# Performance work log

Measured on AMD Instinct MI355X. Metric: run time of the kernel, lower is better.

Reference implementation:

```python
import jax, jax.numpy as jnp
import numpy as np

B, I, D = 2048, 4096, 512          # batch of candidates, num rated items, item_dim
IE, UE = 512, 1024                 # item_emb, user_emb
D1, D2, D3 = 1024, 512, 256        # MLP dense widths


def setup_inputs() -> dict:
    key = jax.random.key(0)
    ks = jax.random.split(key, 16)
    s = 0.02  # weight init scale
    candidate_items = jax.random.normal(ks[0], (B, D), dtype=jnp.float32)
    rated_items = jax.random.normal(ks[1], (I, D), dtype=jnp.float32)
    ratings = jax.random.uniform(ks[2], (B, I), dtype=jnp.float32, minval=0.5, maxval=5.0)
    keep = jax.random.uniform(ks[3], (B, I)) < 0.05
    user_matrix = jnp.where(keep, ratings, 0.0)
    return dict(
        candidate_items=candidate_items,
        rated_items=rated_items,
        user_matrix=user_matrix,
        att_w=jax.random.normal(ks[4], (2 * D, 1), dtype=jnp.float32) * s,
        att_b=jnp.zeros((1,), jnp.float32),
        iw1=jax.random.normal(ks[5], (D, 2 * IE), dtype=jnp.float32) * s,
        ib1=jnp.zeros((2 * IE,), jnp.float32),
        iw2=jax.random.normal(ks[6], (2 * IE, IE), dtype=jnp.float32) * s,
        ib2=jnp.zeros((IE,), jnp.float32),
        uw1=jax.random.normal(ks[7], (D, 2 * UE), dtype=jnp.float32) * s,
        ub1=jnp.zeros((2 * UE,), jnp.float32),
        uw2=jax.random.normal(ks[8], (2 * UE, UE), dtype=jnp.float32) * s,
        ub2=jnp.zeros((UE,), jnp.float32),
        mw1=jax.random.normal(ks[9], (IE + UE, D1), dtype=jnp.float32) * s,
        mb1=jnp.zeros((D1,), jnp.float32),
        mw2=jax.random.normal(ks[10], (D1, D2), dtype=jnp.float32) * s,
        mb2=jnp.zeros((D2,), jnp.float32),
        mw3=jax.random.normal(ks[11], (D2, D3), dtype=jnp.float32) * s,
        mb3=jnp.zeros((D3,), jnp.float32),
        mw4=jax.random.normal(ks[12], (D3, 1), dtype=jnp.float32) * s,
        mb4=jnp.zeros((1,), jnp.float32),
    )


def reference(candidate_items, rated_items, user_matrix,
              att_w, att_b, iw1, ib1, iw2, ib2, uw1, ub1, uw2, ub2,
              mw1, mb1, mw2, mb2, mw3, mb3, mw4, mb4):
    d = candidate_items.shape[1]
    # AttentionNet(Linear(2D,1)) on cat(cand_repeat, rated_tile) decomposes exactly:
    # score[b,i] = cand[b] @ w_c + rated[i] @ w_r + b  (same math, no (B*I,2D) blowup)
    wc, wr = att_w[:d], att_w[d:]                      # (D,1), (D,1)
    scores = candidate_items @ wc + (rated_items @ wr).T + att_b  # (B, I)
    scores = jnp.where(user_matrix == 0.0, -jnp.inf, scores)
    att = jax.nn.softmax(scores, axis=1)
    att = jnp.nan_to_num(att, nan=0.0, posinf=0.0, neginf=0.0)  # rows with no ratings -> 0
    user_feat = (att * user_matrix) @ rated_items      # (B, D)
    # dual towers (dropout = identity in eval)
    item_emb = jax.nn.relu(jax.nn.relu(candidate_items @ iw1 + ib1) @ iw2 + ib2)
    user_emb = jax.nn.relu(jax.nn.relu(user_feat @ uw1 + ub1) @ uw2 + ub2)
    x = jnp.concatenate([item_emb, user_emb], axis=1)  # (B, IE+UE)
    x = jax.nn.relu(x @ mw1 + mb1)
    x = jax.nn.relu(x @ mw2 + mb2)
    x = jax.nn.relu(x @ mw3 + mb3)
    return x @ mw4 + mb4                               # (B, 1)
```

## Files before the change

kernel.cpp:

```cpp
#include <hip/hip_runtime.h>
#include <cstddef>

constexpr int Bn = 2048;
constexpr int In = 4096;
constexpr int Dn = 512;

typedef _Float16 f16;
typedef _Float16 f16x8 __attribute__((ext_vector_type(8)));
typedef float    f32x4 __attribute__((ext_vector_type(4)));

__global__ __launch_bounds__(256) void k_rs(const float* __restrict__ rated,
                                            const float* __restrict__ att_w,
                                            float* __restrict__ rs) {
  const int wid  = threadIdx.x >> 6;
  const int lane = threadIdx.x & 63;
  const int i = blockIdx.x * 4 + wid;
  const float* row = rated + (size_t)i * Dn;
  const float* wr  = att_w + Dn;
  float s = 0.f;
  #pragma unroll
  for (int d = 0; d < Dn / 64; ++d)
    s = fmaf(row[lane + d * 64], wr[lane + d * 64], s);
  #pragma unroll
  for (int off = 32; off > 0; off >>= 1) s += __shfl_down(s, off);
  if (lane == 0) rs[i] = s;
}

__global__ __launch_bounds__(256) void k_att(const float* __restrict__ um,
                                             const float* __restrict__ rs,
                                             f16* __restrict__ att) {
  __shared__ float t[In];
  __shared__ float red[4];
  const int tid = threadIdx.x;
  const int b = blockIdx.x;
  const float* umrow = um + (size_t)b * In;

  float ua[16];
  float lmax = -INFINITY;
  #pragma unroll
  for (int it = 0; it < 4; ++it) {
    const int i = (it * 256 + tid) * 4;
    const float4 v = *reinterpret_cast<const float4*>(umrow + i);
    ua[it * 4 + 0] = v.x; ua[it * 4 + 1] = v.y;
    ua[it * 4 + 2] = v.z; ua[it * 4 + 3] = v.w;
    #pragma unroll
    for (int j = 0; j < 4; ++j) {
      if (ua[it * 4 + j] != 0.f) {
        const float r = rs[i + j];
        t[i + j] = r;
        lmax = fmaxf(lmax, r);
      } else {
        t[i + j] = -INFINITY;
      }
    }
  }
  #pragma unroll
  for (int off = 32; off > 0; off >>= 1) lmax = fmaxf(lmax, __shfl_down(lmax, off));
  if ((tid & 63) == 0) red[tid >> 6] = lmax;
  __syncthreads();
  const float m = fmaxf(fmaxf(red[0], red[1]), fmaxf(red[2], red[3]));
  __syncthreads();

  float lsum = 0.f;
  #pragma unroll
  for (int it = 0; it < 4; ++it) {
    const int i = (it * 256 + tid) * 4;
    #pragma unroll
    for (int j = 0; j < 4; ++j) {
      float v = 0.f;
      if (ua[it * 4 + j] != 0.f) {
        const float e = __expf(t[i + j] - m);
        lsum += e;
        v = e * ua[it * 4 + j];
      }
      t[i + j] = v;
    }
  }
  #pragma unroll
  for (int off = 32; off > 0; off >>= 1) lsum += __shfl_down(lsum, off);
  if ((tid & 63) == 0) red[tid >> 6] = lsum;
  __syncthreads();
  const float S = red[0] + red[1] + red[2] + red[3];
  const float inv = (S > 0.f) ? 1.0f / S : 0.0f;

  f16* arow = att + (size_t)b * In;
  #pragma unroll
  for (int it = 0; it < 2; ++it) {
    const int i = (it * 256 + tid) * 8;
    f16x8 h;
    #pragma unroll
    for (int j = 0; j < 8; ++j) h[j] = (f16)(t[i + j] * inv);
    *reinterpret_cast<f16x8*>(arow + i) = h;
  }
}

struct PrepDesc { const float* src; f16* dst; int K, N, nt, isCast; };
struct PrepPack { PrepDesc d[9]; };

__global__ __launch_bounds__(256) void k_prep(PrepPack pk) {
  __shared__ float tile[32][33];
  int local = blockIdx.x;
  int q = 0;
  while (local >= pk.d[q].nt) { local -= pk.d[q].nt; ++q; }
  const PrepDesc dd = pk.d[q];
  const int tid = threadIdx.x;

  if (dd.isCast) {
    const int i = (local * 256 + tid) * 4;
    const float4 v = *reinterpret_cast<const float4*>(dd.src + i);
    f16* p = dd.dst + i;
    p[0] = (f16)v.x; p[1] = (f16)v.y; p[2] = (f16)v.z; p[3] = (f16)v.w;
    return;
  }
  const int tx = tid & 31;
  const int ty = tid >> 5;
  const int n0 = (local % (dd.N / 32)) * 32;
  const int k0 = (local / (dd.N / 32)) * 32;
  #pragma unroll
  for (int i = 0; i < 4; ++i)
    tile[ty + i * 8][tx] = dd.src[(size_t)(k0 + ty + i * 8) * dd.N + n0 + tx];
  __syncthreads();
  #pragma unroll
  for (int i = 0; i < 4; ++i)
    dd.dst[(size_t)(n0 + ty + i * 8) * dd.K + k0 + tx] = (f16)tile[tx][ty + i * 8];
}

struct GemmDesc {
  const f16* A;
  const f16* Wt;
  const float* bias;
  f16* C;
  float* P;
  int N, K, Kc, ldc, nTilesN, relu;
};

__global__ __launch_bounds__(256) void k_mgemm(GemmDesc dA, GemmDesc dB, int bSplit) {
  const bool second = ((int)blockIdx.x >= bSplit);
  const GemmDesc d = second ? dB : dA;
  const int local = second ? (int)blockIdx.x - bSplit : (int)blockIdx.x;

  const int bm = (local & 15) * 128;
  const int rest = local >> 4;
  const int bn = (rest % d.nTilesN) * 128;
  const int ks = rest / d.nTilesN;
  const int kBeg = ks * d.Kc;

  __shared__ __align__(16) f16 As[128][72];
  __shared__ __align__(16) f16 Bs[128][72];

  const int tid  = threadIdx.x;
  const int lane = tid & 63;
  const int wave = tid >> 6;
  const int wrow = (wave >> 1) * 64;
  const int wcol = (wave & 1) * 64;
  const int lrow = lane & 15;
  const int koff = (lane >> 4) * 8;

  const int ar = tid >> 1;
  const int ac = (tid & 1) * 32;

  const f16* pa = d.A  + (size_t)(bm + ar) * d.K + kBeg + ac;
  const f16* pb = d.Wt + (size_t)(bn + ar) * d.K + kBeg + ac;

  f16x8 ra0, ra1, ra2, ra3, rb0, rb1, rb2, rb3;
  #define LOADG()                                                   \
    ra0 = *reinterpret_cast<const f16x8*>(pa +  0);                 \
    ra1 = *reinterpret_cast<const f16x8*>(pa +  8);                 \
    ra2 = *reinterpret_cast<const f16x8*>(pa + 16);                 \
    ra3 = *reinterpret_cast<const f16x8*>(pa + 24);                 \
    rb0 = *reinterpret_cast<const f16x8*>(pb +  0);                 \
    rb1 = *reinterpret_cast<const f16x8*>(pb +  8);                 \
    rb2 = *reinterpret_cast<const f16x8*>(pb + 16);                 \
    rb3 = *reinterpret_cast<const f16x8*>(pb + 24);

  f32x4 acc[4][4] = {};

  LOADG();
  for (int k0 = 0; k0 < d.Kc; k0 += 64) {
    *reinterpret_cast<f16x8*>(&As[ar][ac +  0]) = ra0;
    *reinterpret_cast<f16x8*>(&As[ar][ac +  8]) = ra1;
    *reinterpret_cast<f16x8*>(&As[ar][ac + 16]) = ra2;
    *reinterpret_cast<f16x8*>(&As[ar][ac + 24]) = ra3;
    *reinterpret_cast<f16x8*>(&Bs[ar][ac +  0]) = rb0;
    *reinterpret_cast<f16x8*>(&Bs[ar][ac +  8]) = rb1;
    *reinterpret_cast<f16x8*>(&Bs[ar][ac + 16]) = rb2;
    *reinterpret_cast<f16x8*>(&Bs[ar][ac + 24]) = rb3;
    __syncthreads();

    if (k0 + 64 < d.Kc) {
      pa += 64; pb += 64;
      LOADG();
    }

    #pragma unroll
    for (int kss = 0; kss < 2; ++kss) {
      const int kk = kss * 32 + koff;
      f16x8 a[4], b[4];
      #pragma unroll
      for (int m = 0; m < 4; ++m)
        a[m] = *reinterpret_cast<const f16x8*>(&As[wrow + m * 16 + lrow][kk]);
      #pragma unroll
      for (int n = 0; n < 4; ++n)
        b[n] = *reinterpret_cast<const f16x8*>(&Bs[wcol + n * 16 + lrow][kk]);
      #pragma unroll
      for (int m = 0; m < 4; ++m)
        #pragma unroll
        for (int n = 0; n < 4; ++n)
          acc[m][n] = __builtin_amdgcn_mfma_f32_16x16x32_f16(a[m], b[n], acc[m][n], 0, 0, 0);
    }
    __syncthreads();
  }
  #undef LOADG

  const int orow = (lane >> 4) * 4;
  if (d.P) {
    float* pp = d.P + (size_t)ks * ((size_t)2048 * d.N);
    #pragma unroll
    for (int mf = 0; mf < 4; ++mf)
      #pragma unroll
      for (int nf = 0; nf < 4; ++nf) {
        const int col = bn + wcol + nf * 16 + lrow;
        #pragma unroll
        for (int rr = 0; rr < 4; ++rr) {
          const int row = bm + wrow + mf * 16 + orow + rr;
          pp[(size_t)row * d.N + col] = acc[mf][nf][rr];
        }
      }
  } else {
    #pragma unroll
    for (int mf = 0; mf < 4; ++mf)
      #pragma unroll
      for (int nf = 0; nf < 4; ++nf) {
        const int col = bn + wcol + nf * 16 + lrow;
        const float bv = d.bias ? d.bias[col] : 0.f;
        #pragma unroll
        for (int rr = 0; rr < 4; ++rr) {
          const int row = bm + wrow + mf * 16 + orow + rr;
          float v = acc[mf][nf][rr] + bv;
          if (d.relu) v = fmaxf(v, 0.f);
          d.C[(size_t)row * d.ldc + col] = (f16)v;
        }
      }
  }
}

struct RedDesc {
  const float* P; int S, MN, N;
  const float* bias; int relu; f16* C; int ldc;
};

__global__ __launch_bounds__(256) void k_reduce2(RedDesc a, RedDesc b, int bSplit) {
  const bool second = ((int)blockIdx.x >= bSplit);
  const RedDesc d = second ? b : a;
  const int local = second ? (int)blockIdx.x - bSplit : (int)blockIdx.x;
  const int idx = (local * 256 + threadIdx.x) * 8;

  float v[8];
  {
    const float4 a0 = *reinterpret_cast<const float4*>(d.P + idx);
    const float4 a1 = *reinterpret_cast<const float4*>(d.P + idx + 4);
    v[0] = a0.x; v[1] = a0.y; v[2] = a0.z; v[3] = a0.w;
    v[4] = a1.x; v[5] = a1.y; v[6] = a1.z; v[7] = a1.w;
  }
  for (int s = 1; s < d.S; ++s) {
    const float* ps = d.P + (size_t)s * d.MN + idx;
    const float4 b0 = *reinterpret_cast<const float4*>(ps);
    const float4 b1 = *reinterpret_cast<const float4*>(ps + 4);
    v[0] += b0.x; v[1] += b0.y; v[2] += b0.z; v[3] += b0.w;
    v[4] += b1.x; v[5] += b1.y; v[6] += b1.z; v[7] += b1.w;
  }
  const int row = idx / d.N;
  const int col = idx % d.N;
  f16x8 h;
  #pragma unroll
  for (int j = 0; j < 8; ++j) {
    float x = v[j] + (d.bias ? d.bias[col + j] : 0.f);
    if (d.relu) x = fmaxf(x, 0.f);
    h[j] = (f16)x;
  }
  *reinterpret_cast<f16x8*>(d.C + (size_t)row * d.ldc + col) = h;
}

__global__ __launch_bounds__(256) void k_tail(const f16* __restrict__ h2,
                                              const f16* __restrict__ t_mw3,
                                              const float* __restrict__ mb3,
                                              const float* __restrict__ mw4,
                                              const float* __restrict__ mb4,
                                              float* __restrict__ out) {
  __shared__ f16 rows[4][512];
  __shared__ float red[4][4];
  const int tid = threadIdx.x;
  const int r0 = blockIdx.x * 4;

  *reinterpret_cast<f16x8*>(&rows[tid >> 6][(tid & 63) * 8]) =
      *reinterpret_cast<const f16x8*>(&h2[(size_t)(r0 + (tid >> 6)) * 512 + (tid & 63) * 8]);
  __syncthreads();

  const int j = tid;
  float acc[4] = {};
  for (int k = 0; k < 512; k += 8) {
    const f16x8 w = *reinterpret_cast<const f16x8*>(&t_mw3[(size_t)j * 512 + k]);
    #pragma unroll
    for (int e = 0; e < 8; ++e) {
      const float wf = (float)w[e];
      #pragma unroll
      for (int r = 0; r < 4; ++r)
        acc[r] = fmaf(wf, (float)rows[r][k + e], acc[r]);
    }
  }
  const float b3 = mb3[j];
  const float m4 = mw4[j];
  const int lane = tid & 63;
  const int wid  = tid >> 6;
  #pragma unroll
  for (int r = 0; r < 4; ++r) {
    float v = fmaxf(acc[r] + b3, 0.f) * m4;
    #pragma unroll
    for (int off = 32; off > 0; off >>= 1) v += __shfl_down(v, off);
    if (lane == 0) red[r][wid] = v;
  }
  __syncthreads();
  if (tid < 4)
    out[r0 + tid] = red[tid][0] + red[tid][1] + red[tid][2] + red[tid][3] + mb4[0];
}

extern "C" void kernel_launch(void* const* d_in, const int* in_sizes, int n_in,
                              void* d_out, int out_size, void* d_ws, size_t ws_size,
                              hipStream_t stream) {
  const float* cand  = (const float*)d_in[0];
  const float* rated = (const float*)d_in[1];
  const float* um    = (const float*)d_in[2];
  const float* att_w = (const float*)d_in[3];
  const float* iw1 = (const float*)d_in[5];
  const float* ib1 = (const float*)d_in[6];
  const float* iw2 = (const float*)d_in[7];
  const float* ib2 = (const float*)d_in[8];
  const float* uw1 = (const float*)d_in[9];
  const float* ub1 = (const float*)d_in[10];
  const float* uw2 = (const float*)d_in[11];
  const float* ub2 = (const float*)d_in[12];
  const float* mw1 = (const float*)d_in[13];
  const float* mb1 = (const float*)d_in[14];
  const float* mw2 = (const float*)d_in[15];
  const float* mb2 = (const float*)d_in[16];
  const float* mw3 = (const float*)d_in[17];
  const float* mb3 = (const float*)d_in[18];
  const float* mw4 = (const float*)d_in[19];
  const float* mb4 = (const float*)d_in[20];
  float* out = (float*)d_out;

  f16*   hws = (f16*)d_ws;
  float* rs  = (float*)d_ws;
  size_t off = 8192;
  auto take = [&](size_t n) { f16* p = hws + off; off += n; return p; };
  f16* t_iw1   = take(512 * 1024);
  f16* t_iw2   = take(1024 * 512);
  f16* t_uw1   = take(512 * 2048);
  f16* t_uw2   = take(2048 * 1024);
  f16* t_mw1   = take(1536 * 1024);
  f16* t_mw2   = take(1024 * 512);
  f16* t_mw3   = take(512 * 256);
  f16* t_rated = take(512 * 4096);
  f16* cand_h  = take(2048 * 512);
  f16* uf_h    = take(2048 * 512);
  f16* big     = take(2048 * 2048);
  f16* Xc      = take(2048 * 1536);
  f16* spare   = take(2048 * 512);
  f16* h_i1b   = take(2048 * 1024);
  float* PA    = (float*)take(4 * 2048 * 512 * 2);
  float* PB    = (float*)take(2 * 2048 * 1024 * 2);
  (void)spare;
  f16* att_d = big;
  f16* h_u1 = big;
  f16* h_m1 = big;
  f16* h_m2 = uf_h;

  dim3 blk(256);

  k_rs<<<dim3(In / 4), blk, 0, stream>>>(rated, att_w, rs);
  PrepPack pk = {{
      { rated, t_rated, 4096,  512, (512/32)*(4096/32), 0 },
      { iw1,   t_iw1,    512, 1024, (1024/32)*(512/32), 0 },
      { iw2,   t_iw2,   1024,  512, (512/32)*(1024/32), 0 },
      { uw1,   t_uw1,    512, 2048, (2048/32)*(512/32), 0 },
      { uw2,   t_uw2,   2048, 1024, (1024/32)*(2048/32), 0 },
      { mw1,   t_mw1,   1536, 1024, (1024/32)*(1536/32), 0 },
      { mw2,   t_mw2,   1024,  512, (512/32)*(1024/32), 0 },
      { mw3,   t_mw3,    512,  256, (256/32)*(512/32), 0 },
      { cand,  cand_h,     0,    0, (Bn * Dn) / 1024, 1 },
  }};
  int prepGrid = 0;
  for (int q = 0; q < 9; ++q) prepGrid += pk.d[q].nt;
  k_prep<<<dim3(prepGrid), blk, 0, stream>>>(pk);
  k_att<<<dim3(Bn), blk, 0, stream>>>(um, rs, att_d);

  GemmDesc dUF = { att_d,  t_rated, nullptr, nullptr, PA, 512, 4096, 1024, 512, 4, 0 };
  GemmDesc dI1 = { cand_h, t_iw1,   nullptr, nullptr, PB, 1024, 512, 256, 1024, 8, 1 };
  GemmDesc dI2 = { h_i1b,  t_iw2,   nullptr, nullptr, PA, 512, 1024, 256, 1536, 4, 1 };
  GemmDesc dU1 = { uf_h,   t_uw1,   ub1, h_u1, nullptr, 2048, 512, 512, 2048, 16, 1 };
  GemmDesc dU2 = { h_u1,   t_uw2,   nullptr, nullptr, PA, 1024, 2048, 1024, 1536, 8, 1 };
  GemmDesc dM1 = { Xc,     t_mw1,   nullptr, nullptr, PA, 1024, 1536, 768, 1024, 8, 1 };
  GemmDesc dM2 = { h_m1,   t_mw2,   nullptr, nullptr, PA, 512, 1024, 256, 512, 4, 1 };

  RedDesc rUF = { PA, 4, 2048 * 512,  512,  nullptr, 0, uf_h,  512 };
  RedDesc rI1 = { PB, 2, 2048 * 1024, 1024, ib1, 1, h_i1b, 1024 };
  RedDesc rI2 = { PA, 4, 2048 * 512,  512,  ib2, 1, Xc,       1536 };
  RedDesc rU2 = { PA, 2, 2048 * 1024, 1024, ub2, 1, Xc + 512, 1536 };
  RedDesc rM1 = { PA, 2, 2048 * 1024, 1024, mb1, 1, h_m1, 1024 };
  RedDesc rM2 = { PA, 4, 2048 * 512,  512,  mb2, 1, h_m2, 512 };

  k_mgemm<<<dim3(512), blk, 0, stream>>>(dUF, dI1, 256);
  k_reduce2<<<dim3(512 + 1024), blk, 0, stream>>>(rUF, rI1, 512);

  k_mgemm<<<dim3(512), blk, 0, stream>>>(dI2, dU1, 256);
  k_reduce2<<<dim3(512), blk, 0, stream>>>(rI2, rI2, 512);

  k_mgemm<<<dim3(256), blk, 0, stream>>>(dU2, dU2, 256);
  k_reduce2<<<dim3(1024), blk, 0, stream>>>(rU2, rU2, 1024);

  k_mgemm<<<dim3(256), blk, 0, stream>>>(dM1, dM1, 256);
  k_reduce2<<<dim3(1024), blk, 0, stream>>>(rM1, rM1, 1024);

  k_mgemm<<<dim3(256), blk, 0, stream>>>(dM2, dM2, 256);
  k_reduce2<<<dim3(512), blk, 0, stream>>>(rM2, rM2, 512);

  k_tail<<<dim3(Bn / 4), blk, 0, stream>>>(h_m2, t_mw3, mb3, mw4, mb4, out);
}
```

Before: 304.1 us.

## Replace split-K GEMMs with 64x64 tiles using direct global-to-LDS loads

The 128x128 split-K GEMM path, which wrote fp32 partials and reduced them in separate kernels, is replaced by a 64x64-tile GEMM that covers the full K and applies bias/ReLU in its epilogue. This removes every reduce kernel and the partial-sum round trips through memory. Tiles are loaded with global_load_lds (direct global-to-shared copies), and the attention and weight-prep kernels are merged into a single launch. In exchange there is less register reuse per tile, no register prefetch double-buffering, and long serial K loops for the K=4096 GEMM.

```diff
diff --git a/kernel.cpp b/kernel.cpp
--- a/kernel.cpp
+++ b/kernel.cpp
@@ -8,6 +8,12 @@
 typedef _Float16 f16;
 typedef _Float16 f16x8 __attribute__((ext_vector_type(8)));
 typedef float    f32x4 __attribute__((ext_vector_type(4)));
+
+__device__ __forceinline__ void gld16(const f16* g, f16* l) {
+  __builtin_amdgcn_global_load_lds(
+      (const __attribute__((address_space(1))) void*)g,
+      (__attribute__((address_space(3))) void*)l, 16, 0, 0);
+}
 
 __global__ __launch_bounds__(256) void k_rs(const float* __restrict__ rated,
                                             const float* __restrict__ att_w,
@@ -26,12 +32,45 @@
   if (lane == 0) rs[i] = s;
 }
 
-__global__ __launch_bounds__(256) void k_att(const float* __restrict__ um,
-                                             const float* __restrict__ rs,
-                                             f16* __restrict__ att) {
-  __shared__ float t[In];
-  __shared__ float red[4];
+struct PrepDesc { const float* src; f16* dst; int K, N, nt, isCast; };
+struct PrepPack { PrepDesc d[9]; };
+
+__global__ __launch_bounds__(256) void k_attprep(const float* __restrict__ um,
+                                                 const float* __restrict__ rs,
+                                                 f16* __restrict__ att,
+                                                 PrepPack pk) {
+  __shared__ float smem[4100];
   const int tid = threadIdx.x;
+
+  if ((int)blockIdx.x >= Bn) {
+    int local = blockIdx.x - Bn;
+    int q = 0;
+    while (local >= pk.d[q].nt) { local -= pk.d[q].nt; ++q; }
+    const PrepDesc dd = pk.d[q];
+    if (dd.isCast) {
+      const int i = (local * 256 + tid) * 4;
+      const float4 v = *reinterpret_cast<const float4*>(dd.src + i);
+      f16* p = dd.dst + i;
+      p[0] = (f16)v.x; p[1] = (f16)v.y; p[2] = (f16)v.z; p[3] = (f16)v.w;
+      return;
+    }
+    float (*tile)[33] = reinterpret_cast<float (*)[33]>(smem);
+    const int tx = tid & 31;
+    const int ty = tid >> 5;
+    const int n0 = (local % (dd.N / 32)) * 32;
+    const int k0 = (local / (dd.N / 32)) * 32;
+    #pragma unroll
+    for (int i = 0; i < 4; ++i)
+      tile[ty + i * 8][tx] = dd.src[(size_t)(k0 + ty + i * 8) * dd.N + n0 + tx];
+    __syncthreads();
+    #pragma unroll
+    for (int i = 0; i < 4; ++i)
+      dd.dst[(size_t)(n0 + ty + i * 8) * dd.K + k0 + tx] = (f16)tile[tx][ty + i * 8];
+    return;
+  }
+
+  float* t = smem;
+  float* red = smem + 4096;
   const int b = blockIdx.x;
   const float* umrow = um + (size_t)b * In;
 
@@ -94,191 +133,86 @@
   }
 }
 
-struct PrepDesc { const float* src; f16* dst; int K, N, nt, isCast; };
-struct PrepPack { PrepDesc d[9]; };
-
-__global__ __launch_bounds__(256) void k_prep(PrepPack pk) {
-  __shared__ float tile[32][33];
-  int local = blockIdx.x;
-  int q = 0;
-  while (local >= pk.d[q].nt) { local -= pk.d[q].nt; ++q; }
-  const PrepDesc dd = pk.d[q];
-  const int tid = threadIdx.x;
-
-  if (dd.isCast) {
-    const int i = (local * 256 + tid) * 4;
-    const float4 v = *reinterpret_cast<const float4*>(dd.src + i);
-    f16* p = dd.dst + i;
-    p[0] = (f16)v.x; p[1] = (f16)v.y; p[2] = (f16)v.z; p[3] = (f16)v.w;
-    return;
-  }
-  const int tx = tid & 31;
-  const int ty = tid >> 5;
-  const int n0 = (local % (dd.N / 32)) * 32;
-  const int k0 = (local / (dd.N / 32)) * 32;
-  #pragma unroll
-  for (int i = 0; i < 4; ++i)
-    tile[ty + i * 8][tx] = dd.src[(size_t)(k0 + ty + i * 8) * dd.N + n0 + tx];
-  __syncthreads();
-  #pragma unroll
-  for (int i = 0; i < 4; ++i)
-    dd.dst[(size_t)(n0 + ty + i * 8) * dd.K + k0 + tx] = (f16)tile[tx][ty + i * 8];
-}
-
 struct GemmDesc {
   const f16* A;
   const f16* Wt;
   const float* bias;
   f16* C;
-  float* P;
-  int N, K, Kc, ldc, nTilesN, relu;
+  int K, ldc, relu;
 };
 
-__global__ __launch_bounds__(256) void k_mgemm(GemmDesc dA, GemmDesc dB, int bSplit) {
+__global__ __launch_bounds__(256, 2) void k_mgemm(GemmDesc dA, GemmDesc dB, int bSplit) {
+  __shared__ __align__(16) f16 As[64 * 64];
+  __shared__ __align__(16) f16 Bs[64 * 64];
+
   const bool second = ((int)blockIdx.x >= bSplit);
   const GemmDesc d = second ? dB : dA;
   const int local = second ? (int)blockIdx.x - bSplit : (int)blockIdx.x;
 
-  const int bm = (local & 15) * 128;
-  const int rest = local >> 4;
-  const int bn = (rest % d.nTilesN) * 128;
-  const int ks = rest / d.nTilesN;
-  const int kBeg = ks * d.Kc;
-
-  __shared__ __align__(16) f16 As[128][72];
-  __shared__ __align__(16) f16 Bs[128][72];
+  const int bm = (local & 31) * 64;
+  const int bn = (local >> 5) * 64;
 
   const int tid  = threadIdx.x;
   const int lane = tid & 63;
   const int wave = tid >> 6;
-  const int wrow = (wave >> 1) * 64;
-  const int wcol = (wave & 1) * 64;
+  const int wrow = (wave >> 1) * 32;
+  const int wcol = (wave & 1) * 32;
   const int lrow = lane & 15;
   const int koff = (lane >> 4) * 8;
 
-  const int ar = tid >> 1;
-  const int ac = (tid & 1) * 32;
-
-  const f16* pa = d.A  + (size_t)(bm + ar) * d.K + kBeg + ac;
-  const f16* pb = d.Wt + (size_t)(bn + ar) * d.K + kBeg + ac;
-
-  f16x8 ra0, ra1, ra2, ra3, rb0, rb1, rb2, rb3;
-  #define LOADG()                                                   \
-    ra0 = *reinterpret_cast<const f16x8*>(pa +  0);                 \
-    ra1 = *reinterpret_cast<const f16x8*>(pa +  8);                 \
-    ra2 = *reinterpret_cast<const f16x8*>(pa + 16);                 \
-    ra3 = *reinterpret_cast<const f16x8*>(pa + 24);                 \
-    rb0 = *reinterpret_cast<const f16x8*>(pb +  0);                 \
-    rb1 = *reinterpret_cast<const f16x8*>(pb +  8);                 \
-    rb2 = *reinterpret_cast<const f16x8*>(pb + 16);                 \
-    rb3 = *reinterpret_cast<const f16x8*>(pb + 24);
-
-  f32x4 acc[4][4] = {};
-
-  LOADG();
-  for (int k0 = 0; k0 < d.Kc; k0 += 64) {
-    *reinterpret_cast<f16x8*>(&As[ar][ac +  0]) = ra0;
-    *reinterpret_cast<f16x8*>(&As[ar][ac +  8]) = ra1;
-    *reinterpret_cast<f16x8*>(&As[ar][ac + 16]) = ra2;
-    *reinterpret_cast<f16x8*>(&As[ar][ac + 24]) = ra3;
-    *reinterpret_cast<f16x8*>(&Bs[ar][ac +  0]) = rb0;
-    *reinterpret_cast<f16x8*>(&Bs[ar][ac +  8]) = rb1;
-    *reinterpret_cast<f16x8*>(&Bs[ar][ac + 16]) = rb2;
-    *reinterpret_cast<f16x8*>(&Bs[ar][ac + 24]) = rb3;
+  const int c0   = wave * 2;
+  const int rgrp = lane >> 3;
+  const int colh = (lane & 7) * 8;
+
+  const f16* gA0 = d.A  + (size_t)(bm + c0 * 8 + rgrp) * d.K + colh;
+  const f16* gA1 = d.A  + (size_t)(bm + c0 * 8 + 8 + rgrp) * d.K + colh;
+  const f16* gB0 = d.Wt + (size_t)(bn + c0 * 8 + rgrp) * d.K + colh;
+  const f16* gB1 = d.Wt + (size_t)(bn + c0 * 8 + 8 + rgrp) * d.K + colh;
+  f16* lA0 = &As[(c0 + 0) * 512];
+  f16* lA1 = &As[(c0 + 1) * 512];
+  f16* lB0 = &Bs[(c0 + 0) * 512];
+  f16* lB1 = &Bs[(c0 + 1) * 512];
+
+  f32x4 acc[2][2] = {};
+
+  for (int k0 = 0; k0 < d.K; k0 += 64) {
+    gld16(gA0 + k0, lA0);
+    gld16(gA1 + k0, lA1);
+    gld16(gB0 + k0, lB0);
+    gld16(gB1 + k0, lB1);
     __syncthreads();
-
-    if (k0 + 64 < d.Kc) {
-      pa += 64; pb += 64;
-      LOADG();
-    }
 
     #pragma unroll
     for (int kss = 0; kss < 2; ++kss) {
       const int kk = kss * 32 + koff;
-      f16x8 a[4], b[4];
+      const f16x8 a0 = *reinterpret_cast<const f16x8*>(&As[(wrow +  0 + lrow) * 64 + kk]);
+      const f16x8 a1 = *reinterpret_cast<const f16x8*>(&As[(wrow + 16 + lrow) * 64 + kk]);
+      const f16x8 b0 = *reinterpret_cast<const f16x8*>(&Bs[(wcol +  0 + lrow) * 64 + kk]);
+      const f16x8 b1 = *reinterpret_cast<const f16x8*>(&Bs[(wcol + 16 + lrow) * 64 + kk]);
+
+      acc[0][0] = __builtin_amdgcn_mfma_f32_16x16x32_f16(a0, b0, acc[0][0], 0, 0, 0);
+      acc[0][1] = __builtin_amdgcn_mfma_f32_16x16x32_f16(a0, b1, acc[0][1], 0, 0, 0);
+      acc[1][0] = __builtin_amdgcn_mfma_f32_16x16x32_f16(a1, b0, acc[1][0], 0, 0, 0);
+      acc[1][1] = __builtin_amdgcn_mfma_f32_16x16x32_f16(a1, b1, acc[1][1], 0, 0, 0);
+    }
+    __syncthreads();
+  }
+
+  const int orow = (lane >> 4) * 4;
+  #pragma unroll
+  for (int mf = 0; mf < 2; ++mf)
+    #pragma unroll
+    for (int nf = 0; nf < 2; ++nf) {
+      const int col = bn + wcol + nf * 16 + lrow;
+      const float bv = d.bias ? d.bias[col] : 0.f;
       #pragma unroll
-      for (int m = 0; m < 4; ++m)
-        a[m] = *reinterpret_cast<const f16x8*>(&As[wrow + m * 16 + lrow][kk]);
-      #pragma unroll
-      for (int n = 0; n < 4; ++n)
-        b[n] = *reinterpret_cast<const f16x8*>(&Bs[wcol + n * 16 + lrow][kk]);
-      #pragma unroll
-      for (int m = 0; m < 4; ++m)
-        #pragma unroll
-        for (int n = 0; n < 4; ++n)
-          acc[m][n] = __builtin_amdgcn_mfma_f32_16x16x32_f16(a[m], b[n], acc[m][n], 0, 0, 0);
-    }
-    __syncthreads();
-  }
-  #undef LOADG
-
-  const int orow = (lane >> 4) * 4;
-  if (d.P) {
-    float* pp = d.P + (size_t)ks * ((size_t)2048 * d.N);
-    #pragma unroll
-    for (int mf = 0; mf < 4; ++mf)
-      #pragma unroll
-      for (int nf = 0; nf < 4; ++nf) {
-        const int col = bn + wcol + nf * 16 + lrow;
-        #pragma unroll
-        for (int rr = 0; rr < 4; ++rr) {
-          const int row = bm + wrow + mf * 16 + orow + rr;
-          pp[(size_t)row * d.N + col] = acc[mf][nf][rr];
-        }
+      for (int rr = 0; rr < 4; ++rr) {
+        const int row = bm + wrow + mf * 16 + orow + rr;
+        float v = acc[mf][nf][rr] + bv;
+        if (d.relu) v = fmaxf(v, 0.f);
+        d.C[(size_t)row * d.ldc + col] = (f16)v;
       }
-  } else {
-    #pragma unroll
-    for (int mf = 0; mf < 4; ++mf)
-      #pragma unroll
-      for (int nf = 0; nf < 4; ++nf) {
-        const int col = bn + wcol + nf * 16 + lrow;
-        const float bv = d.bias ? d.bias[col] : 0.f;
-        #pragma unroll
-        for (int rr = 0; rr < 4; ++rr) {
-          const int row = bm + wrow + mf * 16 + orow + rr;
-          float v = acc[mf][nf][rr] + bv;
-          if (d.relu) v = fmaxf(v, 0.f);
-          d.C[(size_t)row * d.ldc + col] = (f16)v;
-        }
-      }
-  }
-}
-
-struct RedDesc {
-  const float* P; int S, MN, N;
-  const float* bias; int relu; f16* C; int ldc;
-};
-
-__global__ __launch_bounds__(256) void k_reduce2(RedDesc a, RedDesc b, int bSplit) {
-  const bool second = ((int)blockIdx.x >= bSplit);
-  const RedDesc d = second ? b : a;
-  const int local = second ? (int)blockIdx.x - bSplit : (int)blockIdx.x;
-  const int idx = (local * 256 + threadIdx.x) * 8;
-
-  float v[8];
-  {
-    const float4 a0 = *reinterpret_cast<const float4*>(d.P + idx);
-    const float4 a1 = *reinterpret_cast<const float4*>(d.P + idx + 4);
-    v[0] = a0.x; v[1] = a0.y; v[2] = a0.z; v[3] = a0.w;
-    v[4] = a1.x; v[5] = a1.y; v[6] = a1.z; v[7] = a1.w;
-  }
-  for (int s = 1; s < d.S; ++s) {
-    const float* ps = d.P + (size_t)s * d.MN + idx;
-    const float4 b0 = *reinterpret_cast<const float4*>(ps);
-    const float4 b1 = *reinterpret_cast<const float4*>(ps + 4);
-    v[0] += b0.x; v[1] += b0.y; v[2] += b0.z; v[3] += b0.w;
-    v[4] += b1.x; v[5] += b1.y; v[6] += b1.z; v[7] += b1.w;
-  }
-  const int row = idx / d.N;
-  const int col = idx % d.N;
-  f16x8 h;
-  #pragma unroll
-  for (int j = 0; j < 8; ++j) {
-    float x = v[j] + (d.bias ? d.bias[col + j] : 0.f);
-    if (d.relu) x = fmaxf(x, 0.f);
-    h[j] = (f16)x;
-  }
-  *reinterpret_cast<f16x8*>(d.C + (size_t)row * d.ldc + col) = h;
+    }
 }
 
 __global__ __launch_bounds__(256) void k_tail(const f16* __restrict__ h2,
@@ -363,21 +297,17 @@
   f16* t_rated = take(512 * 4096);
   f16* cand_h  = take(2048 * 512);
   f16* uf_h    = take(2048 * 512);
-  f16* big     = take(2048 * 2048);
+  f16* att_d   = take(2048 * 4096);
+  f16* h_i1    = take(2048 * 1024);
   f16* Xc      = take(2048 * 1536);
-  f16* spare   = take(2048 * 512);
-  f16* h_i1b   = take(2048 * 1024);
-  float* PA    = (float*)take(4 * 2048 * 512 * 2);
-  float* PB    = (float*)take(2 * 2048 * 1024 * 2);
-  (void)spare;
-  f16* att_d = big;
-  f16* h_u1 = big;
-  f16* h_m1 = big;
+  f16* h_u1 = att_d;
+  f16* h_m1 = h_i1;
   f16* h_m2 = uf_h;
 
   dim3 blk(256);
 
   k_rs<<<dim3(In / 4), blk, 0, stream>>>(rated, att_w, rs);
+
   PrepPack pk = {{
       { rated, t_rated, 4096,  512, (512/32)*(4096/32), 0 },
       { iw1,   t_iw1,    512, 1024, (1024/32)*(512/32), 0 },
@@ -391,38 +321,21 @@
   }};
   int prepGrid = 0;
   for (int q = 0; q < 9; ++q) prepGrid += pk.d[q].nt;
-  k_prep<<<dim3(prepGrid), blk, 0, stream>>>(pk);
-  k_att<<<dim3(Bn), blk, 0, stream>>>(um, rs, att_d);
-
-  GemmDesc dUF = { att_d,  t_rated, nullptr, nullptr, PA, 512, 4096, 1024, 512, 4, 0 };
-  GemmDesc dI1 = { cand_h, t_iw1,   nullptr, nullptr, PB, 1024, 512, 256, 1024, 8, 1 };
-  GemmDesc dI2 = { h_i1b,  t_iw2,   nullptr, nullptr, PA, 512, 1024, 256, 1536, 4, 1 };
-  GemmDesc dU1 = { uf_h,   t_uw1,   ub1, h_u1, nullptr, 2048, 512, 512, 2048, 16, 1 };
-  GemmDesc dU2 = { h_u1,   t_uw2,   nullptr, nullptr, PA, 1024, 2048, 1024, 1536, 8, 1 };
-  GemmDesc dM1 = { Xc,     t_mw1,   nullptr, nullptr, PA, 1024, 1536, 768, 1024, 8, 1 };
-  GemmDesc dM2 = { h_m1,   t_mw2,   nullptr, nullptr, PA, 512, 1024, 256, 512, 4, 1 };
-
-  RedDesc rUF = { PA, 4, 2048 * 512,  512,  nullptr, 0, uf_h,  512 };
-  RedDesc rI1 = { PB, 2, 2048 * 1024, 1024, ib1, 1, h_i1b, 1024 };
-  RedDesc rI2 = { PA, 4, 2048 * 512,  512,  ib2, 1, Xc,       1536 };
-  RedDesc rU2 = { PA, 2, 2048 * 1024, 1024, ub2, 1, Xc + 512, 1536 };
-  RedDesc rM1 = { PA, 2, 2048 * 1024, 1024, mb1, 1, h_m1, 1024 };
-  RedDesc rM2 = { PA, 4, 2048 * 512,  512,  mb2, 1, h_m2, 512 };
-
-  k_mgemm<<<dim3(512), blk, 0, stream>>>(dUF, dI1, 256);
-  k_reduce2<<<dim3(512 + 1024), blk, 0, stream>>>(rUF, rI1, 512);
-
-  k_mgemm<<<dim3(512), blk, 0, stream>>>(dI2, dU1, 256);
-  k_reduce2<<<dim3(512), blk, 0, stream>>>(rI2, rI2, 512);
-
-  k_mgemm<<<dim3(256), blk, 0, stream>>>(dU2, dU2, 256);
-  k_reduce2<<<dim3(1024), blk, 0, stream>>>(rU2, rU2, 1024);
-
-  k_mgemm<<<dim3(256), blk, 0, stream>>>(dM1, dM1, 256);
-  k_reduce2<<<dim3(1024), blk, 0, stream>>>(rM1, rM1, 1024);
-
+  k_attprep<<<dim3(Bn + prepGrid), blk, 0, stream>>>(um, rs, att_d, pk);
+
+  GemmDesc dUF = { att_d,  t_rated, nullptr, uf_h,     4096,  512, 0 };
+  GemmDesc dI1 = { cand_h, t_iw1,   ib1,     h_i1,      512, 1024, 1 };
+  GemmDesc dU1 = { uf_h,   t_uw1,   ub1,     h_u1,      512, 2048, 1 };
+  GemmDesc dI2 = { h_i1,   t_iw2,   ib2,     Xc,       1024, 1536, 1 };
+  GemmDesc dU2 = { h_u1,   t_uw2,   ub2,     Xc + 512, 2048, 1536, 1 };
+  GemmDesc dM1 = { Xc,     t_mw1,   mb1,     h_m1,     1536, 1024, 1 };
+  GemmDesc dM2 = { h_m1,   t_mw2,   mb2,     h_m2,     1024,  512, 1 };
+
+  k_mgemm<<<dim3(768), blk, 0, stream>>>(dUF, dI1, 256);
+  k_mgemm<<<dim3(1280), blk, 0, stream>>>(dU1, dI2, 1024);
+  k_mgemm<<<dim3(512), blk, 0, stream>>>(dU2, dU2, 512);
+  k_mgemm<<<dim3(512), blk, 0, stream>>>(dM1, dM1, 512);
   k_mgemm<<<dim3(256), blk, 0, stream>>>(dM2, dM2, 256);
-  k_reduce2<<<dim3(512), blk, 0, stream>>>(rM2, rM2, 512);
 
   k_tail<<<dim3(Bn / 4), blk, 0, stream>>>(h_m2, t_mw3, mb3, mw4, mb4, out);
 }
```

Measured after the change: 300.7 us. No clear change (-1.1%).
